# Optimization experiments

Hardware: AMD Instinct MI355X
Metric: run time of the kernel (lower is better)

The kernel has to match this reference:

```python
import jax, jax.numpy as jnp
import numpy as np

EPS = 1e-10


def setup_inputs() -> dict:
    key = jax.random.key(0)
    k1, k2, k3 = jax.random.split(key, 3)
    B, X, Y = 16, 512, 512
    predictions = jax.random.uniform(k1, (B, 5, X, Y), dtype=jnp.float32)
    inputs = jax.random.uniform(k2, (B, 3, X, Y), dtype=jnp.float32)
    heart = jax.random.randint(k3, (B, 1, X, Y), 0, 2, dtype=jnp.int32)
    return {"predictions": predictions, "inputs": inputs, "heart": heart}


def reference(predictions, inputs, heart):
    # predictions: [B,5,X,Y] soft class maps (chan 0 unused); inputs: [B,3,X,Y] MRI modalities
    # heart: [B,1,X,Y] binary ROI mask. Loops over b/k/m in the torch source are vectorized;
    # boolean-mask gathers become multiply-by-mask with masked reductions (same math).
    mask = (heart[:, 0] == 1).astype(predictions.dtype)          # [B,X,Y]
    pred = predictions[:, 1:5]                                   # [B,K=4,X,Y]
    inp = inputs                                                 # [B,M=3,X,Y]

    w = pred * mask[:, None]                                     # masked soft weights [B,K,X,Y]
    sw = jnp.sum(w, axis=(2, 3))                                 # [B,K]
    denom = sw[:, :, None] + EPS                                 # [B,K,1]

    # per-(k,m) weighted mean over masked pixels
    mu = jnp.einsum('bkxy,bmxy->bkm', w, inp) / denom            # [B,K,M]
    diff = inp[:, None, :, :, :] - mu[:, :, :, None, None]       # [B,K,M,X,Y]
    var = jnp.einsum('bkxy,bkmxy->bkm', w, diff * diff) / denom + EPS

    # Gaussian pdf per (k,m,pixel), scaled by pred_k (as in temp[k,m] = pred[k]*pdf)
    inv_norm = 1.0 / jnp.sqrt(2.0 * jnp.pi * var)                # [B,K,M]
    pdf = inv_norm[:, :, :, None, None] * jnp.exp(
        -(diff * diff) / (2.0 * var)[:, :, :, None, None])      # [B,K,M,X,Y]
    temp = pred[:, :, None] * pdf                                # [B,K,M,X,Y]

    mix = jnp.sum(jnp.prod(temp, axis=2), axis=1)                # [B,X,Y]
    loglik = jnp.log(mix + EPS)                                  # [B,X,Y]

    # masked mean over ROI pixels per batch (== torch.mean over gathered pixels)
    per_b = -jnp.sum(loglik * mask, axis=(1, 2)) / jnp.sum(mask, axis=(1, 2))
    return jnp.mean(per_b)
```

## Files before the change

### kernel.cpp

```cpp
#include <hip/hip_runtime.h>
#include <math.h>
#include <stdint.h>

constexpr int NB  = 16;
constexpr int XY  = 512 * 512;
constexpr int NV  = XY / 4;

constexpr int G1  = 32;
constexpr int WIN = 256;
constexpr int NIT = NV / (G1 * WIN);
constexpr int NPL = 8;
static_assert((NIT & 1) == 0, "LDS-reuse epilogue assumes last window lives in buf1");

constexpr int P1OFF = 4096;
constexpr int P2OFF = P1OFF + NB * G1 * 32 * 4;

__device__ __forceinline__ float waveReduce64(float v) {
#pragma unroll
    for (int off = 32; off > 0; off >>= 1) v += __shfl_down(v, off, 64);
    return v;
}

__device__ __forceinline__ float rfl(float x) {
    return __uint_as_float(__builtin_amdgcn_readfirstlane(__float_as_uint(x)));
}

__device__ __forceinline__ void gl2lds(const void* g, void* l) {
    __builtin_amdgcn_global_load_lds(
        (__attribute__((address_space(1))) void*)(void*)g,
        (__attribute__((address_space(3))) void*)l,
        16, 0, 0);
}

#define PIX1(h_, e0_, e1_, e2_, p0_, p1_, p2_, p3_) do {                      \
    float mm_ = ((h_) == 1) ? 1.f : 0.f;                                      \
    cnt += mm_;                                                               \
    float w0_ = (p0_) * mm_, w1_ = (p1_) * mm_, w2_ = (p2_) * mm_,            \
          w3_ = (p3_) * mm_;                                                  \
    s0_0 += w0_; s0_1 += w1_; s0_2 += w2_; s0_3 += w3_;                       \
    float t_;                                                                 \
    t_ = w0_ * (e0_); u00 += t_; q00 = fmaf(t_, (e0_), q00);                  \
    t_ = w0_ * (e1_); u01 += t_; q01 = fmaf(t_, (e1_), q01);                  \
    t_ = w0_ * (e2_); u02 += t_; q02 = fmaf(t_, (e2_), q02);                  \
    t_ = w1_ * (e0_); u10 += t_; q10 = fmaf(t_, (e0_), q10);                  \
    t_ = w1_ * (e1_); u11 += t_; q11 = fmaf(t_, (e1_), q11);                  \
    t_ = w1_ * (e2_); u12 += t_; q12 = fmaf(t_, (e2_), q12);                  \
    t_ = w2_ * (e0_); u20 += t_; q20 = fmaf(t_, (e0_), q20);                  \
    t_ = w2_ * (e1_); u21 += t_; q21 = fmaf(t_, (e1_), q21);                  \
    t_ = w2_ * (e2_); u22 += t_; q22 = fmaf(t_, (e2_), q22);                  \
    t_ = w3_ * (e0_); u30 += t_; q30 = fmaf(t_, (e0_), q30);                  \
    t_ = w3_ * (e1_); u31 += t_; q31 = fmaf(t_, (e1_), q31);                  \
    t_ = w3_ * (e2_); u32 += t_; q32 = fmaf(t_, (e2_), q32);                  \
} while (0)

#define PARAMK(K_, mu0_, mu1_, mu2_, h0_, h1_, h2_, C_) {                     \
    double S0_ = tot[1 + (K_)];                                               \
    double den_ = S0_ + 1e-10;                                                \
    double Cd_ = 1.0;                                                         \
    double S1_, S2_, muv_, var_;                                              \
    S1_ = tot[5 + (K_)*3 + 0]; S2_ = tot[17 + (K_)*3 + 0];                    \
    muv_ = S1_ / den_;                                                        \
    var_ = (S2_ - 2.0 * muv_ * S1_ + muv_ * muv_ * S0_) / den_ + 1e-10;       \
    mu0_ = (float)muv_; h0_ = (float)(0.5 / var_);                            \
    Cd_ *= 1.0 / sqrt(6.283185307179586 * var_);                              \
    S1_ = tot[5 + (K_)*3 + 1]; S2_ = tot[17 + (K_)*3 + 1];                    \
    muv_ = S1_ / den_;                                                        \
    var_ = (S2_ - 2.0 * muv_ * S1_ + muv_ * muv_ * S0_) / den_ + 1e-10;       \
    mu1_ = (float)muv_; h1_ = (float)(0.5 / var_);                            \
    Cd_ *= 1.0 / sqrt(6.283185307179586 * var_);                              \
    S1_ = tot[5 + (K_)*3 + 2]; S2_ = tot[17 + (K_)*3 + 2];                    \
    muv_ = S1_ / den_;                                                        \
    var_ = (S2_ - 2.0 * muv_ * S1_ + muv_ * muv_ * S0_) / den_ + 1e-10;       \
    mu2_ = (float)muv_; h2_ = (float)(0.5 / var_);                            \
    Cd_ *= 1.0 / sqrt(6.283185307179586 * var_);                              \
    C_ = (float)Cd_;                                                          \
}

#define PIX2(h_, e0_, e1_, e2_, p0_, p1_, p2_, p3_) do {                      \
    float m_ = ((h_) == 1) ? 1.f : 0.f;                                       \
    float d0_, d1_, d2_, ex_, pc_;                                            \
    float mix_;                                                               \
    d0_ = (e0_) - mu00; d1_ = (e1_) - mu01; d2_ = (e2_) - mu02;               \
    ex_ = fmaf(d0_ * d0_, hv00, fmaf(d1_ * d1_, hv01, d2_ * d2_ * hv02));     \
    pc_ = (p0_) * (p0_) * (p0_);                                              \
    mix_ = C0 * pc_ * __expf(-ex_);                                           \
    d0_ = (e0_) - mu10; d1_ = (e1_) - mu11; d2_ = (e2_) - mu12;               \
    ex_ = fmaf(d0_ * d0_, hv10, fmaf(d1_ * d1_, hv11, d2_ * d2_ * hv12));     \
    pc_ = (p1_) * (p1_) * (p1_);                                              \
    mix_ = fmaf(C1 * pc_, __expf(-ex_), mix_);                                \
    d0_ = (e0_) - mu20; d1_ = (e1_) - mu21; d2_ = (e2_) - mu22;               \
    ex_ = fmaf(d0_ * d0_, hv20, fmaf(d1_ * d1_, hv21, d2_ * d2_ * hv22));     \
    pc_ = (p2_) * (p2_) * (p2_);                                              \
    mix_ = fmaf(C2 * pc_, __expf(-ex_), mix_);                                \
    d0_ = (e0_) - mu30; d1_ = (e1_) - mu31; d2_ = (e2_) - mu32;               \
    ex_ = fmaf(d0_ * d0_, hv30, fmaf(d1_ * d1_, hv31, d2_ * d2_ * hv32));     \
    pc_ = (p3_) * (p3_) * (p3_);                                              \
    mix_ = fmaf(C3 * pc_, __expf(-ex_), mix_);                                \
    lacc += m_ * __logf(mix_ + 1e-10f);                                       \
} while (0)

#define STAGE(B_, IT_) do {                                                   \
    const size_t o_ = (size_t)(IT_) * 4096;                                   \
    char* lb_ = lds + (B_) * (NPL * 4096) + wav * 1024;                       \
    gl2lds(gH  + o_, lb_ + 0 * 4096);                                         \
    gl2lds(gI0 + o_, lb_ + 1 * 4096);                                         \
    gl2lds(gI1 + o_, lb_ + 2 * 4096);                                         \
    gl2lds(gI2 + o_, lb_ + 3 * 4096);                                         \
    gl2lds(gP1 + o_, lb_ + 4 * 4096);                                         \
    gl2lds(gP2 + o_, lb_ + 5 * 4096);                                         \
    gl2lds(gP3 + o_, lb_ + 6 * 4096);                                         \
    gl2lds(gP4 + o_, lb_ + 7 * 4096);                                         \
} while (0)

#define LOADREGS(B_)                                                          \
    const char* cb_ = lds + (B_) * (NPL * 4096);                              \
    int4   h  = *(const int4*)  (cb_ + 0 * 4096 + tid * 16);                  \
    float4 f0 = *(const float4*)(cb_ + 1 * 4096 + tid * 16);                  \
    float4 f1 = *(const float4*)(cb_ + 2 * 4096 + tid * 16);                  \
    float4 f2 = *(const float4*)(cb_ + 3 * 4096 + tid * 16);                  \
    float4 g0 = *(const float4*)(cb_ + 4 * 4096 + tid * 16);                  \
    float4 g1 = *(const float4*)(cb_ + 5 * 4096 + tid * 16);                  \
    float4 g2 = *(const float4*)(cb_ + 6 * 4096 + tid * 16);                  \
    float4 g3 = *(const float4*)(cb_ + 7 * 4096 + tid * 16);

#define DECL_GSRC                                                             \
    const char* Pb = (const char*)(predictions + (size_t)b * 5 * XY);         \
    const char* Ib = (const char*)(inputs      + (size_t)b * 3 * XY);         \
    const char* Hb = (const char*)(heart       + (size_t)b * XY);             \
    const size_t vb = (size_t)(g * (NIT * WIN) + wav * 64 + lane) * 16;       \
    const char* gH  = Hb + vb;                                                \
    const char* gI0 = Ib + 0 * (size_t)XY * 4 + vb;                           \
    const char* gI1 = Ib + 1 * (size_t)XY * 4 + vb;                           \
    const char* gI2 = Ib + 2 * (size_t)XY * 4 + vb;                           \
    const char* gP1 = Pb + 1 * (size_t)XY * 4 + vb;                           \
    const char* gP2 = Pb + 2 * (size_t)XY * 4 + vb;                           \
    const char* gP3 = Pb + 3 * (size_t)XY * 4 + vb;                           \
    const char* gP4 = Pb + 4 * (size_t)XY * 4 + vb;

#define WAIT_LGKM  asm volatile("s_waitcnt lgkmcnt(0)" ::: "memory")
#define WAIT_VM    asm volatile("s_waitcnt vmcnt(0)"   ::: "memory")

__global__ __launch_bounds__(256) void pass1_moments(
        const float* __restrict__ predictions,
        const float* __restrict__ inputs,
        const int*   __restrict__ heart,
        char*        __restrict__ wsraw) {
    const int b    = blockIdx.y;
    const int g    = blockIdx.x;
    const int tid  = threadIdx.x;
    const int lane = tid & 63;
    const int wav  = tid >> 6;

    __shared__ __align__(16) char lds[2 * NPL * 4096];

    DECL_GSRC;

    float cnt = 0.f;
    float s0_0 = 0.f, s0_1 = 0.f, s0_2 = 0.f, s0_3 = 0.f;
    float u00 = 0.f, u01 = 0.f, u02 = 0.f, u10 = 0.f, u11 = 0.f, u12 = 0.f;
    float u20 = 0.f, u21 = 0.f, u22 = 0.f, u30 = 0.f, u31 = 0.f, u32 = 0.f;
    float q00 = 0.f, q01 = 0.f, q02 = 0.f, q10 = 0.f, q11 = 0.f, q12 = 0.f;
    float q20 = 0.f, q21 = 0.f, q22 = 0.f, q30 = 0.f, q31 = 0.f, q32 = 0.f;

    STAGE(0, 0);
    WAIT_VM;
    for (int it = 0; it < NIT; ++it) {
        LOADREGS(it & 1);
        WAIT_LGKM;
        if (it + 1 < NIT) STAGE((it + 1) & 1, it + 1);
        PIX1(h.x, f0.x, f1.x, f2.x, g0.x, g1.x, g2.x, g3.x);
        PIX1(h.y, f0.y, f1.y, f2.y, g0.y, g1.y, g2.y, g3.y);
        PIX1(h.z, f0.z, f1.z, f2.z, g0.z, g1.z, g2.z, g3.z);
        PIX1(h.w, f0.w, f1.w, f2.w, g0.w, g1.w, g2.w, g3.w);
        WAIT_VM;
    }

    __syncthreads();
    float* shred = reinterpret_cast<float*>(lds);
#define REDS(i_, var_) { float r_ = waveReduce64(var_); if (lane == 0) shred[wav * 32 + (i_)] = r_; }
    REDS(0, cnt);
    REDS(1, s0_0); REDS(2, s0_1); REDS(3, s0_2); REDS(4, s0_3);
    REDS(5, u00); REDS(6, u01); REDS(7, u02);
    REDS(8, u10); REDS(9, u11); REDS(10, u12);
    REDS(11, u20); REDS(12, u21); REDS(13, u22);
    REDS(14, u30); REDS(15, u31); REDS(16, u32);
    REDS(17, q00); REDS(18, q01); REDS(19, q02);
    REDS(20, q10); REDS(21, q11); REDS(22, q12);
    REDS(23, q20); REDS(24, q21); REDS(25, q22);
    REDS(26, q30); REDS(27, q31); REDS(28, q32);
#undef REDS
    __syncthreads();
    if (tid < 29) {
        float v = shred[tid] + shred[32 + tid] + shred[64 + tid] + shred[96 + tid];
        float* p1 = reinterpret_cast<float*>(wsraw + P1OFF);
        p1[(((size_t)b * G1 + g) << 5) + tid] = v;
    }
}

__global__ __launch_bounds__(256) void reduce_totals(char* __restrict__ wsraw) {
    const int b   = blockIdx.x;
    const int tid = threadIdx.x;
    const float* p1 = reinterpret_cast<const float*>(wsraw + P1OFF) + ((size_t)b * G1 << 5);
    __shared__ double red[8][32];
    const int col = tid & 31, r = tid >> 5;
    double s = 0.0;
    if (col < 29) {
#pragma unroll
        for (int j = r; j < G1; j += 8) s += (double)p1[((size_t)j << 5) + col];
    }
    red[r][col] = s;
    __syncthreads();
    if (tid < 29) {
        double t = 0.0;
#pragma unroll
        for (int r2 = 0; r2 < 8; ++r2) t += red[r2][tid];
        reinterpret_cast<double*>(wsraw)[(size_t)b * 32 + tid] = t;
    }
}

__global__ __launch_bounds__(256) void pass2_loglik(
        const float* __restrict__ predictions,
        const float* __restrict__ inputs,
        const int*   __restrict__ heart,
        char*        __restrict__ wsraw) {
    const int b    = blockIdx.y;
    const int g    = blockIdx.x;
    const int tid  = threadIdx.x;
    const int lane = tid & 63;
    const int wav  = tid >> 6;

    __shared__ __align__(16) char lds[2 * NPL * 4096];

    const double* tot = reinterpret_cast<const double*>(wsraw) + (size_t)b * 32;

    float mu00, mu01, mu02, mu10, mu11, mu12, mu20, mu21, mu22, mu30, mu31, mu32;
    float hv00, hv01, hv02, hv10, hv11, hv12, hv20, hv21, hv22, hv30, hv31, hv32;
    float C0, C1, C2, C3;
    PARAMK(0, mu00, mu01, mu02, hv00, hv01, hv02, C0);
    PARAMK(1, mu10, mu11, mu12, hv10, hv11, hv12, C1);
    PARAMK(2, mu20, mu21, mu22, hv20, hv21, hv22, C2);
    PARAMK(3, mu30, mu31, mu32, hv30, hv31, hv32, C3);
    mu00=rfl(mu00); mu01=rfl(mu01); mu02=rfl(mu02);
    mu10=rfl(mu10); mu11=rfl(mu11); mu12=rfl(mu12);
    mu20=rfl(mu20); mu21=rfl(mu21); mu22=rfl(mu22);
    mu30=rfl(mu30); mu31=rfl(mu31); mu32=rfl(mu32);
    hv00=rfl(hv00); hv01=rfl(hv01); hv02=rfl(hv02);
    hv10=rfl(hv10); hv11=rfl(hv11); hv12=rfl(hv12);
    hv20=rfl(hv20); hv21=rfl(hv21); hv22=rfl(hv22);
    hv30=rfl(hv30); hv31=rfl(hv31); hv32=rfl(hv32);
    C0=rfl(C0); C1=rfl(C1); C2=rfl(C2); C3=rfl(C3);

    DECL_GSRC;

    float lacc = 0.f;

    STAGE(0, 0);
    WAIT_VM;
    for (int it = 0; it < NIT; ++it) {
        LOADREGS(it & 1);
        WAIT_LGKM;
        if (it + 1 < NIT) STAGE((it + 1) & 1, it + 1);
        PIX2(h.x, f0.x, f1.x, f2.x, g0.x, g1.x, g2.x, g3.x);
        PIX2(h.y, f0.y, f1.y, f2.y, g0.y, g1.y, g2.y, g3.y);
        PIX2(h.z, f0.z, f1.z, f2.z, g0.z, g1.z, g2.z, g3.z);
        PIX2(h.w, f0.w, f1.w, f2.w, g0.w, g1.w, g2.w, g3.w);
        WAIT_VM;
    }

    __syncthreads();
    float* shred = reinterpret_cast<float*>(lds);
    {
        float v = waveReduce64(lacc);
        if (lane == 0) shred[wav] = v;
    }
    __syncthreads();
    if (tid == 0) {
        float* p2 = reinterpret_cast<float*>(wsraw + P2OFF);
        p2[(size_t)b * G1 + g] = shred[0] + shred[1] + shred[2] + shred[3];
    }
}

__global__ __launch_bounds__(256) void finalize_kernel(
        const char* __restrict__ wsraw, float* __restrict__ out) {
    const float*  p2  = reinterpret_cast<const float*>(wsraw + P2OFF);
    const double* tot = reinterpret_cast<const double*>(wsraw);
    __shared__ double red[16][17];
    const int tid = threadIdx.x;
    const int b = tid >> 4, r = tid & 15;
    double s = 0.0;
#pragma unroll
    for (int j = r; j < G1; j += 16)
        s += (double)p2[(size_t)b * G1 + j];
    red[b][r] = s;
    __syncthreads();
    double v = 0.0;
    if (tid < NB) {
        double l = 0.0;
#pragma unroll
        for (int r2 = 0; r2 < 16; ++r2) l += red[tid][r2];
        v = -l / tot[(size_t)tid * 32];
    }
#pragma unroll
    for (int off = 8; off > 0; off >>= 1) v += __shfl_down(v, off, 64);
    if (tid == 0) out[0] = (float)(v / (double)NB);
}

extern "C" void kernel_launch(void* const* d_in, const int* in_sizes, int n_in,
                              void* d_out, int out_size, void* d_ws, size_t ws_size,
                              hipStream_t stream) {
    const float* predictions = (const float*)d_in[0];
    const float* inputs      = (const float*)d_in[1];
    const int*   heart       = (const int*)d_in[2];
    float* out   = (float*)d_out;
    char*  wsraw = (char*)d_ws;

    pass1_moments<<<dim3(G1, NB), 256, 0, stream>>>(predictions, inputs, heart, wsraw);
    reduce_totals<<<dim3(NB),     256, 0, stream>>>(wsraw);
    pass2_loglik <<<dim3(G1, NB), 256, 0, stream>>>(predictions, inputs, heart, wsraw);
    finalize_kernel<<<1,          256, 0, stream>>>(wsraw, out);
}
```

Measured before the change: 194.8 us.

## Restructure LDS staging: per-wave plane ownership with two-deep prefetch and barriers

Each wave now loads whole 4 KB slabs of two planes (heart or one input channel, plus one prediction channel) into LDS. Before, every wave loaded a 1 KB slice of all eight planes. The loop keeps two windows in flight using vmcnt(8) partial waits and workgroup barriers instead of a full vmcnt(0) drain each iteration. This is meant to hide global-to-LDS latency better and make each wave's accesses more contiguous. In exchange it adds two s_barriers per window, so every wave depends on the other waves' loads.

Result: slower. 205.0 us (+5.2%).

```diff
diff --git a/kernel.cpp b/kernel.cpp
--- a/kernel.cpp
+++ b/kernel.cpp
@@ -6,11 +6,10 @@
 constexpr int XY  = 512 * 512;
 constexpr int NV  = XY / 4;
 
-constexpr int G1  = 32;
-constexpr int WIN = 256;
-constexpr int NIT = NV / (G1 * WIN);
-constexpr int NPL = 8;
-static_assert((NIT & 1) == 0, "LDS-reuse epilogue assumes last window lives in buf1");
+constexpr int G1   = 32;
+constexpr int WIN  = 256;
+constexpr int NWIN = NV / (G1 * WIN);
+constexpr int BUFB = 8 * 4096;
 
 constexpr int P1OFF = 4096;
 constexpr int P2OFF = P1OFF + NB * G1 * 32 * 4;
@@ -31,6 +30,11 @@
         (__attribute__((address_space(3))) void*)l,
         16, 0, 0);
 }
+
+#define VMWAIT8  do { asm volatile("s_waitcnt vmcnt(8)" ::: "memory"); \
+                      __builtin_amdgcn_sched_barrier(0); } while (0)
+#define VMWAIT0  do { asm volatile("s_waitcnt vmcnt(0)" ::: "memory"); \
+                      __builtin_amdgcn_sched_barrier(0); } while (0)
 
 #define PIX1(h_, e0_, e1_, e2_, p0_, p1_, p2_, p3_) do {                      \
     float mm_ = ((h_) == 1) ? 1.f : 0.f;                                      \
@@ -99,21 +103,22 @@
     lacc += m_ * __logf(mix_ + 1e-10f);                                       \
 } while (0)
 
-#define STAGE(B_, IT_) do {                                                   \
-    const size_t o_ = (size_t)(IT_) * 4096;                                   \
-    char* lb_ = lds + (B_) * (NPL * 4096) + wav * 1024;                       \
-    gl2lds(gH  + o_, lb_ + 0 * 4096);                                         \
-    gl2lds(gI0 + o_, lb_ + 1 * 4096);                                         \
-    gl2lds(gI1 + o_, lb_ + 2 * 4096);                                         \
-    gl2lds(gI2 + o_, lb_ + 3 * 4096);                                         \
-    gl2lds(gP1 + o_, lb_ + 4 * 4096);                                         \
-    gl2lds(gP2 + o_, lb_ + 5 * 4096);                                         \
-    gl2lds(gP3 + o_, lb_ + 6 * 4096);                                         \
-    gl2lds(gP4 + o_, lb_ + 7 * 4096);                                         \
+#define STAGE(B_, W_) do {                                                    \
+    const size_t go_ = (size_t)(W_) * 4096;                                   \
+    char* dA_ = lds + (B_) * BUFB + wav * 4096;                               \
+    char* dB_ = dA_ + 4 * 4096;                                               \
+    gl2lds(gA + go_ +    0, dA_ +    0);                                      \
+    gl2lds(gA + go_ + 1024, dA_ + 1024);                                      \
+    gl2lds(gA + go_ + 2048, dA_ + 2048);                                      \
+    gl2lds(gA + go_ + 3072, dA_ + 3072);                                      \
+    gl2lds(gB + go_ +    0, dB_ +    0);                                      \
+    gl2lds(gB + go_ + 1024, dB_ + 1024);                                      \
+    gl2lds(gB + go_ + 2048, dB_ + 2048);                                      \
+    gl2lds(gB + go_ + 3072, dB_ + 3072);                                      \
 } while (0)
 
 #define LOADREGS(B_)                                                          \
-    const char* cb_ = lds + (B_) * (NPL * 4096);                              \
+    const char* cb_ = lds + (B_) * BUFB;                                      \
     int4   h  = *(const int4*)  (cb_ + 0 * 4096 + tid * 16);                  \
     float4 f0 = *(const float4*)(cb_ + 1 * 4096 + tid * 16);                  \
     float4 f1 = *(const float4*)(cb_ + 2 * 4096 + tid * 16);                  \
@@ -124,21 +129,25 @@
     float4 g3 = *(const float4*)(cb_ + 7 * 4096 + tid * 16);
 
 #define DECL_GSRC                                                             \
-    const char* Pb = (const char*)(predictions + (size_t)b * 5 * XY);         \
-    const char* Ib = (const char*)(inputs      + (size_t)b * 3 * XY);         \
-    const char* Hb = (const char*)(heart       + (size_t)b * XY);             \
-    const size_t vb = (size_t)(g * (NIT * WIN) + wav * 64 + lane) * 16;       \
-    const char* gH  = Hb + vb;                                                \
-    const char* gI0 = Ib + 0 * (size_t)XY * 4 + vb;                           \
-    const char* gI1 = Ib + 1 * (size_t)XY * 4 + vb;                           \
-    const char* gI2 = Ib + 2 * (size_t)XY * 4 + vb;                           \
-    const char* gP1 = Pb + 1 * (size_t)XY * 4 + vb;                           \
-    const char* gP2 = Pb + 2 * (size_t)XY * 4 + vb;                           \
-    const char* gP3 = Pb + 3 * (size_t)XY * 4 + vb;                           \
-    const char* gP4 = Pb + 4 * (size_t)XY * 4 + vb;
-
-#define WAIT_LGKM  asm volatile("s_waitcnt lgkmcnt(0)" ::: "memory")
-#define WAIT_VM    asm volatile("s_waitcnt vmcnt(0)"   ::: "memory")
+    const size_t slab_ = (size_t)g * (NWIN * WIN) * 16 + (size_t)lane * 16;   \
+    const char* gA = (wav == 0)                                               \
+        ? (const char*)heart + (size_t)b * XY * 4 + slab_                     \
+        : (const char*)inputs + ((size_t)b * 3 + (wav - 1)) * XY * 4 + slab_; \
+    const char* gB = (const char*)predictions                                 \
+        + ((size_t)b * 5 + (wav + 1)) * XY * 4 + slab_;
+
+#define STREAM_LOOP(PIXSET_)                                                  \
+    STAGE(0, 0);                                                              \
+    STAGE(1, 1);                                                              \
+    _Pragma("unroll")                                                         \
+    for (int w = 0; w < NWIN; ++w) {                                          \
+        if (w < NWIN - 1) { VMWAIT8; } else { VMWAIT0; }                      \
+        __builtin_amdgcn_s_barrier();   \
+        LOADREGS(w & 1);                                                      \
+        PIXSET_;                                                              \
+        __builtin_amdgcn_s_barrier();   \
+        if (w + 2 < NWIN) STAGE(w & 1, w + 2);                                \
+    }
 
 __global__ __launch_bounds__(256) void pass1_moments(
         const float* __restrict__ predictions,
@@ -151,7 +160,8 @@
     const int lane = tid & 63;
     const int wav  = tid >> 6;
 
-    __shared__ __align__(16) char lds[2 * NPL * 4096];
+    __shared__ __align__(16) char lds[2 * BUFB];
+    __shared__ float shred[4][32];
 
     DECL_GSRC;
 
@@ -162,22 +172,16 @@
     float q00 = 0.f, q01 = 0.f, q02 = 0.f, q10 = 0.f, q11 = 0.f, q12 = 0.f;
     float q20 = 0.f, q21 = 0.f, q22 = 0.f, q30 = 0.f, q31 = 0.f, q32 = 0.f;
 
-    STAGE(0, 0);
-    WAIT_VM;
-    for (int it = 0; it < NIT; ++it) {
-        LOADREGS(it & 1);
-        WAIT_LGKM;
-        if (it + 1 < NIT) STAGE((it + 1) & 1, it + 1);
-        PIX1(h.x, f0.x, f1.x, f2.x, g0.x, g1.x, g2.x, g3.x);
-        PIX1(h.y, f0.y, f1.y, f2.y, g0.y, g1.y, g2.y, g3.y);
-        PIX1(h.z, f0.z, f1.z, f2.z, g0.z, g1.z, g2.z, g3.z);
-        PIX1(h.w, f0.w, f1.w, f2.w, g0.w, g1.w, g2.w, g3.w);
-        WAIT_VM;
-    }
-
-    __syncthreads();
-    float* shred = reinterpret_cast<float*>(lds);
-#define REDS(i_, var_) { float r_ = waveReduce64(var_); if (lane == 0) shred[wav * 32 + (i_)] = r_; }
+#define PIXSET1_                                                              \
+    PIX1(h.x, f0.x, f1.x, f2.x, g0.x, g1.x, g2.x, g3.x);                      \
+    PIX1(h.y, f0.y, f1.y, f2.y, g0.y, g1.y, g2.y, g3.y);                      \
+    PIX1(h.z, f0.z, f1.z, f2.z, g0.z, g1.z, g2.z, g3.z);                      \
+    PIX1(h.w, f0.w, f1.w, f2.w, g0.w, g1.w, g2.w, g3.w)
+
+    STREAM_LOOP(PIXSET1_);
+
+    __syncthreads();
+#define REDS(i_, var_) { float r_ = waveReduce64(var_); if (lane == 0) shred[wav][i_] = r_; }
     REDS(0, cnt);
     REDS(1, s0_0); REDS(2, s0_1); REDS(3, s0_2); REDS(4, s0_3);
     REDS(5, u00); REDS(6, u01); REDS(7, u02);
@@ -191,7 +195,7 @@
 #undef REDS
     __syncthreads();
     if (tid < 29) {
-        float v = shred[tid] + shred[32 + tid] + shred[64 + tid] + shred[96 + tid];
+        float v = shred[0][tid] + shred[1][tid] + shred[2][tid] + shred[3][tid];
         float* p1 = reinterpret_cast<float*>(wsraw + P1OFF);
         p1[(((size_t)b * G1 + g) << 5) + tid] = v;
     }
@@ -229,7 +233,8 @@
     const int lane = tid & 63;
     const int wav  = tid >> 6;
 
-    __shared__ __align__(16) char lds[2 * NPL * 4096];
+    __shared__ __align__(16) char lds[2 * BUFB];
+    __shared__ float shred2[4];
 
     const double* tot = reinterpret_cast<const double*>(wsraw) + (size_t)b * 32;
 
@@ -254,29 +259,23 @@
 
     float lacc = 0.f;
 
-    STAGE(0, 0);
-    WAIT_VM;
-    for (int it = 0; it < NIT; ++it) {
-        LOADREGS(it & 1);
-        WAIT_LGKM;
-        if (it + 1 < NIT) STAGE((it + 1) & 1, it + 1);
-        PIX2(h.x, f0.x, f1.x, f2.x, g0.x, g1.x, g2.x, g3.x);
-        PIX2(h.y, f0.y, f1.y, f2.y, g0.y, g1.y, g2.y, g3.y);
-        PIX2(h.z, f0.z, f1.z, f2.z, g0.z, g1.z, g2.z, g3.z);
-        PIX2(h.w, f0.w, f1.w, f2.w, g0.w, g1.w, g2.w, g3.w);
-        WAIT_VM;
-    }
-
-    __syncthreads();
-    float* shred = reinterpret_cast<float*>(lds);
+#define PIXSET2_                                                              \
+    PIX2(h.x, f0.x, f1.x, f2.x, g0.x, g1.x, g2.x, g3.x);                      \
+    PIX2(h.y, f0.y, f1.y, f2.y, g0.y, g1.y, g2.y, g3.y);                      \
+    PIX2(h.z, f0.z, f1.z, f2.z, g0.z, g1.z, g2.z, g3.z);                      \
+    PIX2(h.w, f0.w, f1.w, f2.w, g0.w, g1.w, g2.w, g3.w)
+
+    STREAM_LOOP(PIXSET2_);
+
+    __syncthreads();
     {
         float v = waveReduce64(lacc);
-        if (lane == 0) shred[wav] = v;
+        if (lane == 0) shred2[wav] = v;
     }
     __syncthreads();
     if (tid == 0) {
         float* p2 = reinterpret_cast<float*>(wsraw + P2OFF);
-        p2[(size_t)b * G1 + g] = shred[0] + shred[1] + shred[2] + shred[3];
+        p2[(size_t)b * G1 + g] = shred2[0] + shred2[1] + shred2[2] + shred2[3];
     }
 }
 
```
